# Optimization experiments

Measured on AMD Instinct MI355X. Metric: run time of the kernel, lower is better.

## Reference

```python
import jax, jax.numpy as jnp
import numpy as np

LNC = -1000000000.0
B, K, L, V, D = 64, 8, 256, 50257, 1024
EOS, PAD = 50256, 0
LENGTH_PENALTY = 1.0
EARLY_STOPPING = False


def _gather_beams(t, idx):
    # t: (B, old_beams, ...), idx: (B, new_beams) -> (B, new_beams, ...)
    idx = idx.reshape(idx.shape + (1,) * (t.ndim - 2))
    return jnp.take_along_axis(t, idx, axis=1)


def setup_inputs() -> dict:
    key = jax.random.key(0)
    ks = jax.random.split(key, 8)
    return dict(
        input_ids=jax.random.randint(ks[0], (B * K, 1), 0, V).astype(jnp.int32),
        sequences_state=jax.random.randint(ks[1], (B, K, L), 0, V).astype(jnp.int32),
        running_sequences_state=jax.random.randint(ks[2], (B, K, L), 0, V).astype(jnp.int32),
        log_probs_state=jax.random.normal(ks[3], (B, K), jnp.float32),
        running_log_probs_state=jax.random.normal(ks[4], (B, K), jnp.float32),
        is_finished_state=jax.random.randint(ks[5], (B, K), 0, 2).astype(jnp.int32),
        embed=jax.random.normal(ks[6], (V, D), jnp.float32) * 0.02,
        W=jax.random.normal(ks[7], (D, V), jnp.float32) * 0.02,
        absolute_step=17,
    )


def reference(input_ids, sequences_state, running_sequences_state, log_probs_state,
              running_log_probs_state, is_finished_state, embed, W, absolute_step):
    step = absolute_step  # static python int (current decode position)
    # mask selecting slot 0 for the freshly fed token
    mask = jnp.zeros((B, K, L), jnp.int32).at[:, :, 0].set(1)
    padded = jnp.pad(input_ids, ((0, 0), (0, L - 1))).reshape(B, K, L)
    running_sequences = mask * padded + (1 - mask) * running_sequences_state  # (B,K,L) int32

    # model: embedding lookup + LM head GEMM on the token at step-1
    model_input_ids = running_sequences[:, :, step - 1].reshape(B * K)
    logits = embed[model_input_ids] @ W                      # (B*K, V)
    log_probs = jax.nn.log_softmax(logits, axis=-1)          # logits_processor = identity
    log_probs = log_probs.reshape(B, K, V) + running_log_probs_state[:, :, None]
    flat = log_probs.reshape(B, K * V)

    beams_to_keep = 2 * K
    topk_log_probs, topk_indices = jax.lax.top_k(flat, beams_to_keep)  # (B,2K)
    topk_beam_indices = topk_indices // V
    topk_running_sequences = _gather_beams(running_sequences, topk_beam_indices)  # (B,2K,L)
    topk_ids = (topk_indices % V).astype(jnp.int32)
    topk_sequences = topk_running_sequences.at[:, :, step].set(topk_ids)

    did_finish = topk_sequences[:, :, step] == EOS           # (B,2K) bool
    running_topk_log_probs = topk_log_probs + did_finish * LNC
    next_topk_indices = jax.lax.top_k(running_topk_log_probs, K)[1]
    next_running_sequences = _gather_beams(topk_sequences, next_topk_indices)      # (B,K,L)
    next_running_log_probs = _gather_beams(running_topk_log_probs, next_topk_indices)

    topk_log_probs = topk_log_probs / (step ** LENGTH_PENALTY)
    full = jnp.all(is_finished_state.astype(bool), axis=-1, keepdims=True) & (EARLY_STOPPING is True)
    add_penalty = (~did_finish) | full
    topk_log_probs = topk_log_probs + add_penalty * LNC

    merged_sequences = jnp.concatenate([sequences_state, topk_sequences], axis=1)      # (B,3K,L)
    merged_log_probs = jnp.concatenate([log_probs_state, topk_log_probs], axis=1)      # (B,3K)
    merged_is_finished = jnp.concatenate([is_finished_state.astype(bool), did_finish], axis=1)
    topk_merged_indices = jax.lax.top_k(merged_log_probs, K)[1]
    next_sequences = _gather_beams(merged_sequences, topk_merged_indices)
    next_log_probs = _gather_beams(merged_log_probs, topk_merged_indices)
    next_is_finished = _gather_beams(merged_is_finished, topk_merged_indices)

    not_max_length_yet = step < L
    worst_finished = jnp.where(jnp.any(next_is_finished, axis=1),
                               jnp.min(log_probs_state, axis=1),
                               jnp.full((B,), LNC, jnp.float32))
    best_running = running_log_probs_state[:, 0] / (step ** LENGTH_PENALTY)
    improvement = jnp.any(best_running > worst_finished)
    still_open = ~(jnp.all(next_is_finished) & (EARLY_STOPPING is True))
    continue_search = not_max_length_yet & still_open & improvement

    none_finished = jnp.any(next_is_finished, axis=1)
    seqs = jnp.where(none_finished[:, None, None], next_sequences, next_running_sequences)
    generated_tokens = seqs[:, 0]                 # (B, L)
    done = ~continue_search
    return generated_tokens, done, next_log_probs, next_running_log_probs
```

## Files before the change

kernel.cpp:

```cpp
#include <hip/hip_runtime.h>
#include <cstdint>
#include <cstddef>

#define BB 64
#define KK 8
#define LL 256
#define VV 50257
#define DD 1024
#define EOS_TOK 50256
#define LNCf (-1000000000.0f)
#define NT 393
#define NCOL 50304
#define MAXT 400

typedef unsigned short ushort_t;
typedef __attribute__((ext_vector_type(4))) float f32x4;
typedef __attribute__((ext_vector_type(8))) short bf16x8;

struct __attribute__((packed, aligned(4))) f4u { float x, y, z, w; };

__device__ inline ushort_t bf16_rne(float x) {
    unsigned u = __float_as_uint(x);
    return (ushort_t)((u + 0x7fffu + ((u >> 16) & 1u)) >> 16);
}
__device__ inline float bf16_f32(ushort_t b) { return __uint_as_float(((unsigned)b) << 16); }

__global__ __launch_bounds__(256) void conv_aw(
    const float* __restrict__ embed, const int* __restrict__ input_ids,
    const int* __restrict__ rss, const int* __restrict__ step_p,
    ushort_t* __restrict__ At_hi, ushort_t* __restrict__ At_lo,
    const float* __restrict__ W, ushort_t* __restrict__ Wt)
{
    __shared__ ushort_t tile[64][66];
    const int bx = blockIdx.x;
    const int t = threadIdx.x;

    if (bx < 512) {
        const int r = bx;
        const int step = *step_p;
        const int tok = (step == 1) ? input_ids[r] : rss[r * LL + (step - 1)];
        f32x4 v = *(const f32x4*)(embed + (size_t)tok * DD + t * 4);
        ushort4 h, l;
        h.x = bf16_rne(v[0]); l.x = bf16_rne(v[0] - bf16_f32(h.x));
        h.y = bf16_rne(v[1]); l.y = bf16_rne(v[1] - bf16_f32(h.y));
        h.z = bf16_rne(v[2]); l.z = bf16_rne(v[2] - bf16_f32(h.z));
        h.w = bf16_rne(v[3]); l.w = bf16_rne(v[3] - bf16_f32(h.w));
        *(ushort4*)(At_hi + (size_t)r * DD + t * 4) = h;
        *(ushort4*)(At_lo + (size_t)r * DD + t * 4) = l;
        return;
    }

    const int b2 = bx - 512;
    const int k0 = (b2 & 15) * 64;
    const int n0 = (b2 >> 4) * 64;
    const int kr = t >> 4;
    const int nc = (t & 15) * 4;
#pragma unroll
    for (int j = 0; j < 4; ++j) {
        const int k = k0 + kr + j * 16;
        const int n = n0 + nc;
        const float* wp = W + (size_t)k * VV + n;
        float a, b3, c, d;
        if (n + 3 < VV) { f4u u = *(const f4u*)wp; a = u.x; b3 = u.y; c = u.z; d = u.w; }
        else {
            a  = (n     < VV) ? wp[0] : 0.f;
            b3 = (n + 1 < VV) ? wp[1] : 0.f;
            c  = (n + 2 < VV) ? wp[2] : 0.f;
            d  = (n + 3 < VV) ? wp[3] : 0.f;
        }
        tile[kr + j * 16][nc + 0] = bf16_rne(a);
        tile[kr + j * 16][nc + 1] = bf16_rne(b3);
        tile[kr + j * 16][nc + 2] = bf16_rne(c);
        tile[kr + j * 16][nc + 3] = bf16_rne(d);
    }
    __syncthreads();
    const int nr = t >> 2;
    const int kc = (t & 3) * 16;
    ushort_t vals[16];
#pragma unroll
    for (int j = 0; j < 16; ++j) vals[j] = tile[kc + j][nr];
    uint4 u0, u1;
    u0.x = vals[0] | ((unsigned)vals[1] << 16);  u0.y = vals[2] | ((unsigned)vals[3] << 16);
    u0.z = vals[4] | ((unsigned)vals[5] << 16);  u0.w = vals[6] | ((unsigned)vals[7] << 16);
    u1.x = vals[8] | ((unsigned)vals[9] << 16);  u1.y = vals[10] | ((unsigned)vals[11] << 16);
    u1.z = vals[12] | ((unsigned)vals[13] << 16); u1.w = vals[14] | ((unsigned)vals[15] << 16);
    ushort_t* op = Wt + (size_t)(n0 + nr) * DD + k0 + kc;
    *(uint4*)op = u0;
    *(uint4*)(op + 8) = u1;
}

__global__ __launch_bounds__(256) void gemm_full(
    const ushort_t* __restrict__ At_hi, const ushort_t* __restrict__ At_lo,
    const ushort_t* __restrict__ Wt, float* __restrict__ logits,
    float* __restrict__ msum)
{
    __shared__ ushort_t smem[24576];
    ushort_t* Ah = smem;
    ushort_t* Al = smem + 8192;
    ushort_t* Bs = smem + 16384;

    const int tid = threadIdx.x;
    const int wave = tid >> 6;
    const int lane = tid & 63;
    const int i = blockIdx.x;
    const int m_t = (i >> 3) & 3;
    const int n_t = (i & 7) + (((i >> 3) >> 2) << 3);
    if (n_t >= NT) return;
    const int m0 = m_t * 128;
    const int wm = wave >> 1, wn = wave & 1;
    const int fr = lane & 15;
    const int q  = lane >> 4;

    const int srow = lane >> 3;
    const int schunk = lane & 7;

    f32x4 acc[4][4];
#pragma unroll
    for (int a = 0; a < 4; ++a)
#pragma unroll
        for (int b = 0; b < 4; ++b)
#pragma unroll
            for (int e = 0; e < 4; ++e) acc[a][b][e] = 0.f;

    for (int t7 = 0; t7 < 16; ++t7) {
        const int kb = t7 * 64;
#pragma unroll
        for (int ii = 0; ii < 4; ++ii) {
            const int row = (ii * 4 + wave) * 8 + srow;
            const int soff = (schunk ^ (row & 7)) * 8;
            const ushort_t* srcH = At_hi + (size_t)(m0 + row) * DD + kb + soff;
            const ushort_t* srcL = At_lo + (size_t)(m0 + row) * DD + kb + soff;
            const ushort_t* srcB = Wt + (size_t)(n_t * 128 + row) * DD + kb + soff;
            __builtin_amdgcn_global_load_lds(
                (const __attribute__((address_space(1))) unsigned int*)srcH,
                (__attribute__((address_space(3))) unsigned int*)(Ah + (ii * 4 + wave) * 512),
                16, 0, 0);
            __builtin_amdgcn_global_load_lds(
                (const __attribute__((address_space(1))) unsigned int*)srcL,
                (__attribute__((address_space(3))) unsigned int*)(Al + (ii * 4 + wave) * 512),
                16, 0, 0);
            __builtin_amdgcn_global_load_lds(
                (const __attribute__((address_space(1))) unsigned int*)srcB,
                (__attribute__((address_space(3))) unsigned int*)(Bs + (ii * 4 + wave) * 512),
                16, 0, 0);
        }
        __syncthreads();
#pragma unroll
        for (int h = 0; h < 2; ++h) {
            bf16x8 b[4];
#pragma unroll
            for (int fn = 0; fn < 4; ++fn) {
                const int row = wn * 64 + fn * 16 + fr;
                const int off = ((h * 4 + q) ^ (row & 7)) * 16;
                b[fn] = *(const bf16x8*)((const char*)(Bs + row * 64) + off);
            }
#pragma unroll
            for (int fm = 0; fm < 4; ++fm) {
                const int row = wm * 64 + fm * 16 + fr;
                const int off = ((h * 4 + q) ^ (row & 7)) * 16;
                bf16x8 ah = *(const bf16x8*)((const char*)(Ah + row * 64) + off);
                bf16x8 al = *(const bf16x8*)((const char*)(Al + row * 64) + off);
#pragma unroll
                for (int fn = 0; fn < 4; ++fn) {
                    acc[fm][fn] = __builtin_amdgcn_mfma_f32_16x16x32_bf16(ah, b[fn], acc[fm][fn], 0, 0, 0);
                    acc[fm][fn] = __builtin_amdgcn_mfma_f32_16x16x32_bf16(al, b[fn], acc[fm][fn], 0, 0, 0);
                }
            }
        }
        __syncthreads();
    }

    const int n0 = n_t * 128;
    if (n0 + 128 > VV) {
        const int cgb = n0 + wn * 64 + fr;
#pragma unroll
        for (int fn = 0; fn < 4; ++fn)
            if (cgb + fn * 16 >= VV) {
#pragma unroll
                for (int fm = 0; fm < 4; ++fm)
#pragma unroll
                    for (int e = 0; e < 4; ++e) acc[fm][fn][e] = -INFINITY;
            }
    }

    const int crow0 = m0 + wm * 64 + q * 4;
    const int ccol0 = n0 + wn * 64 + fr;
#pragma unroll
    for (int fm = 0; fm < 4; ++fm)
#pragma unroll
        for (int fn = 0; fn < 4; ++fn) {
            const int col = ccol0 + fn * 16;
#pragma unroll
            for (int e = 0; e < 4; ++e)
                logits[(size_t)(crow0 + fm * 16 + e) * NCOL + col] = acc[fm][fn][e];
        }

    float* msb = (float*)smem;
#pragma unroll
    for (int fm = 0; fm < 4; ++fm)
#pragma unroll
        for (int e = 0; e < 4; ++e) {
            const float v0 = acc[fm][0][e], v1 = acc[fm][1][e];
            const float v2 = acc[fm][2][e], v3 = acc[fm][3][e];
            float vm = fmaxf(fmaxf(v0, v1), fmaxf(v2, v3));
#pragma unroll
            for (int sh = 1; sh < 16; sh <<= 1) vm = fmaxf(vm, __shfl_xor(vm, sh, 64));
            float vs = __expf(v0 - vm) + __expf(v1 - vm) + __expf(v2 - vm) + __expf(v3 - vm);
#pragma unroll
            for (int sh = 1; sh < 16; sh <<= 1) vs += __shfl_xor(vs, sh, 64);
            if (fr == 0) {
                const int row = wm * 64 + fm * 16 + q * 4 + e;
                msb[row * 4 + wn * 2]     = vm;
                msb[row * 4 + wn * 2 + 1] = vs;
            }
        }
    __syncthreads();
    if (tid < 128) {
        const float M0 = msb[tid * 4], S0 = msb[tid * 4 + 1];
        const float M1 = msb[tid * 4 + 2], S1 = msb[tid * 4 + 3];
        const float M = fmaxf(M0, M1);
        const float S = S0 * __expf(M0 - M) + S1 * __expf(M1 - M);
        const size_t p = (size_t)(m0 + tid) * NT + n_t;
        msum[p * 2] = M; msum[p * 2 + 1] = S;
    }
}

__global__ __launch_bounds__(64) void prune_scan(
    const float* __restrict__ msum, float* __restrict__ lse_out,
    int* __restrict__ tlist, int* __restrict__ tcount)
{
    const int r = blockIdx.x;
    const int lane = threadIdx.x;

    float m = -INFINITY, s = 0.f;
    float tv[16]; int tvi[16];
#pragma unroll
    for (int j = 0; j < 16; ++j) { tv[j] = -INFINITY; tvi[j] = 0x7fffffff; }

    for (int p = lane; p < NT; p += 64) {
        const size_t pb = (size_t)r * NT + p;
        const float M = msum[pb * 2], S = msum[pb * 2 + 1];
        const float mm = fmaxf(m, M);
        s = s * __expf(m - mm) + S * __expf(M - mm);
        m = mm;
        if (M > tv[15]) {
            float cv = M; int ci = p;
#pragma unroll
            for (int j = 0; j < 16; ++j) {
                const bool sw = (cv > tv[j]);
                const float tf = tv[j]; const int ti2 = tvi[j];
                if (sw) { tv[j] = cv; tvi[j] = ci; cv = tf; ci = ti2; }
            }
        }
    }
#pragma unroll
    for (int sh = 1; sh < 64; sh <<= 1) {
        const float m2 = __shfl_xor(m, sh, 64), s2 = __shfl_xor(s, sh, 64);
        const float mm = fmaxf(m, m2);
        s = s * __expf(m - mm) + s2 * __expf(m2 - mm);
        m = mm;
    }
    if (lane == 0) lse_out[r] = m + logf(s);

    unsigned used = 0;
    float T = -INFINITY;
#pragma unroll
    for (int t = 0; t < 16; ++t) {
        float bv = -INFINITY; int bi = 0x7fffffff;
#pragma unroll
        for (int j = 0; j < 16; ++j) {
            if (!((used >> j) & 1u) &&
                (tv[j] > bv || (tv[j] == bv && tvi[j] < bi))) { bv = tv[j]; bi = tvi[j]; }
        }
#pragma unroll
        for (int sh = 1; sh < 64; sh <<= 1) {
            const float v2 = __shfl_xor(bv, sh, 64);
            const int i2 = __shfl_xor(bi, sh, 64);
            if (v2 > bv || (v2 == bv && i2 < bi)) { bv = v2; bi = i2; }
        }
#pragma unroll
        for (int j = 0; j < 16; ++j)
            if (tvi[j] == bi) used |= 1u << j;
        T = bv;
    }

    __shared__ int cnt;
    if (lane == 0) cnt = 0;
    __syncthreads();
    for (int p = lane; p < NT; p += 64) {
        const float M = msum[((size_t)r * NT + p) * 2];
        if (M >= T) {
            const int slot = atomicAdd(&cnt, 1);
            tlist[r * MAXT + slot] = p;
        }
    }
    __syncthreads();
    if (lane == 0) tcount[r] = cnt;
}

__global__ __launch_bounds__(256) void topk_sparse(
    const float* __restrict__ logits, const int* __restrict__ tlist,
    const int* __restrict__ tcount, float* __restrict__ tv_out,
    int* __restrict__ ti_out)
{
    const int r = blockIdx.x;
    const int tid = threadIdx.x;
    const int cnt = tcount[r];

    float v[16]; int id[16];
#pragma unroll
    for (int j = 0; j < 16; ++j) { v[j] = -INFINITY; id[j] = 0x7fffffff; }

    const int total = cnt * 128;
    for (int idx = tid; idx < total; idx += 256) {
        const int tile = tlist[r * MAXT + (idx >> 7)];
        const int col = tile * 128 + (idx & 127);
        const float x = logits[(size_t)r * NCOL + col];
        if (x > v[15] || (x == v[15] && col < id[15])) {
            float cv = x; int ci = col;
#pragma unroll
            for (int j = 0; j < 16; ++j) {
                const bool sw = (cv > v[j]) || (cv == v[j] && ci < id[j]);
                const float tf = v[j]; const int ti2 = id[j];
                if (sw) { v[j] = cv; id[j] = ci; cv = tf; ci = ti2; }
            }
        }
    }

    __shared__ float mvv[256][17];
    __shared__ int mii[256][17];
#pragma unroll
    for (int j = 0; j < 16; ++j) { mvv[tid][j] = v[j]; mii[tid][j] = id[j]; }
    __syncthreads();

    auto level = [&](int st) {
        float nv[16]; int ni2[16];
        const float* av = mvv[tid];      const int* ai = mii[tid];
        const float* bv = mvv[tid + st]; const int* bi = mii[tid + st];
        int pa = 0, pb = 0;
#pragma unroll
        for (int o = 0; o < 16; ++o) {
            const float va = av[pa], vb2 = bv[pb];
            const int ia = ai[pa], ib = bi[pb];
            const bool ta = (va > vb2) || (va == vb2 && ia < ib);
            nv[o] = ta ? va : vb2;
            ni2[o] = ta ? ia : ib;
            pa += ta ? 1 : 0;
            pb += ta ? 0 : 1;
        }
#pragma unroll
        for (int j = 0; j < 16; ++j) { mvv[tid][j] = nv[j]; mii[tid][j] = ni2[j]; }
    };

    if (tid < 128) level(128);
    __syncthreads();
    if (tid < 64) {
        level(64); level(32); level(16); level(8); level(4); level(2); level(1);
        if (tid < 16) {
            tv_out[r * 16 + tid] = mvv[0][tid];
            ti_out[r * 16 + tid] = mii[0][tid];
        }
    }
}

__global__ __launch_bounds__(64) void beam_logic(
    const float* __restrict__ lse, const float* __restrict__ tv,
    const int* __restrict__ ti, const int* __restrict__ input_ids,
    const int* __restrict__ seq_state, const int* __restrict__ rss,
    const float* __restrict__ lps, const float* __restrict__ rlps,
    const int* __restrict__ isfin, const int* __restrict__ step_p,
    float* __restrict__ out, int* __restrict__ improve_ws)
{
    const int b = blockIdx.x;
    const int lane = threadIdx.x;
    const int kk = lane >> 3;
    const int r = b * KK + kk;

    const float off_r = rlps[r] - lse[r];

    const int s0 = (lane & 7) * 2;
    float cv[2]; int cidx[2];
#pragma unroll
    for (int mq = 0; mq < 2; ++mq) {
        cv[mq] = tv[r * 16 + s0 + mq] + off_r;
        cidx[mq] = kk * VV + ti[r * 16 + s0 + mq];
    }

    float wv[16]; int wi[16];
#pragma unroll
    for (int t = 0; t < 16; ++t) {
        float bv = cv[0]; int bi = cidx[0];
        if (cv[1] > bv || (cv[1] == bv && cidx[1] < bi)) { bv = cv[1]; bi = cidx[1]; }
#pragma unroll
        for (int sh = 1; sh < 64; sh <<= 1) {
            const float v2 = __shfl_xor(bv, sh, 64);
            const int i2 = __shfl_xor(bi, sh, 64);
            if (v2 > bv || (v2 == bv && i2 < bi)) { bv = v2; bi = i2; }
        }
        wv[t] = bv; wi[t] = bi;
#pragma unroll
        for (int mq = 0; mq < 2; ++mq)
            if (cidx[mq] == bi) { cv[mq] = -INFINITY; cidx[mq] = 0x7fffffff; }
    }

    int mode = 0, beam = 0, selk = 0, selv = 0, step = 0;
    if (lane == 0) {
        step = *step_p;
        const float stepf = (float)step;
        float runtl[16]; int tkk[16], tkid[16]; unsigned finmask = 0;
#pragma unroll
        for (int j = 0; j < 16; ++j) {
            tkk[j] = wi[j] / VV;
            tkid[j] = wi[j] - tkk[j] * VV;
            const bool f = (tkid[j] == EOS_TOK);
            finmask |= (f ? 1u : 0u) << j;
            runtl[j] = wv[j] + (f ? LNCf : 0.f);
        }
        unsigned used = 0;
        int selk_run = 0, selv_run = 0;
#pragma unroll
        for (int i2 = 0; i2 < 8; ++i2) {
            float bvv = 0.f; int bj = -1, bk = 0, bv2 = 0;
#pragma unroll
            for (int j = 0; j < 16; ++j) {
                if (!((used >> j) & 1u) && (bj < 0 || runtl[j] > bvv)) {
                    bvv = runtl[j]; bj = j; bk = tkk[j]; bv2 = tkid[j];
                }
            }
            used |= 1u << bj;
            out[BB * LL + 1 + BB * KK + b * KK + i2] = bvv;
            if (i2 == 0) { selk_run = bk; selv_run = bv2; }
        }
        float mvx[24]; unsigned mfinmask = 0;
#pragma unroll
        for (int j = 0; j < 8; ++j) {
            mvx[j] = lps[b * KK + j];
            mfinmask |= ((isfin[b * KK + j] != 0) ? 1u : 0u) << j;
        }
#pragma unroll
        for (int j = 0; j < 16; ++j) {
            const bool f = (finmask >> j) & 1u;
            mvx[8 + j] = wv[j] / stepf + (f ? 0.f : LNCf);
            mfinmask |= (f ? 1u : 0u) << (8 + j);
        }
        unsigned used2 = 0; int anyf = 0;
        int m0_state = 0, m0_beam = 0, m0_k = 0, m0_v = 0;
#pragma unroll
        for (int i2 = 0; i2 < 8; ++i2) {
            float bvv = 0.f; int bj = -1, bf = 0, bstate = 0, bbeam = 0, bk = 0, bv2 = 0;
#pragma unroll
            for (int j = 0; j < 24; ++j) {
                if (!((used2 >> j) & 1u) && (bj < 0 || mvx[j] > bvv)) {
                    bvv = mvx[j]; bj = j; bf = (mfinmask >> j) & 1u;
                    bstate = (j < 8) ? 1 : 0; bbeam = j;
                    bk = (j < 8) ? 0 : tkk[j - 8]; bv2 = (j < 8) ? 0 : tkid[j - 8];
                }
            }
            used2 |= 1u << bj;
            out[BB * LL + 1 + b * KK + i2] = bvv;
            anyf |= bf;
            if (i2 == 0) { m0_state = bstate; m0_beam = bbeam; m0_k = bk; m0_v = bv2; }
        }
        float worst = LNCf;
        if (anyf) {
            worst = lps[b * KK];
#pragma unroll
            for (int j = 1; j < 8; ++j) worst = fminf(worst, lps[b * KK + j]);
        }
        improve_ws[b] = ((rlps[b * KK] / stepf) > worst) ? 1 : 0;
        if (anyf) {
            if (m0_state) { mode = 0; beam = m0_beam; }
            else { mode = 1; selk = m0_k; selv = m0_v; }
        } else {
            mode = 1; selk = selk_run; selv = selv_run;
        }
    }
    mode = __shfl(mode, 0, 64);
    beam = __shfl(beam, 0, 64);
    selk = __shfl(selk, 0, 64);
    selv = __shfl(selv, 0, 64);
    step = __shfl(step, 0, 64);

#pragma unroll
    for (int it = 0; it < 4; ++it) {
        const int t2 = it * 64 + lane;
        int tokv;
        if (mode == 0) {
            tokv = seq_state[(b * KK + beam) * LL + t2];
        } else {
            tokv = (t2 == step) ? selv
                 : ((t2 == 0) ? input_ids[b * KK + selk]
                              : rss[(b * KK + selk) * LL + t2]);
        }
        out[b * LL + t2] = (float)tokv;
    }
}

__global__ __launch_bounds__(64) void finalize_done(
    const int* __restrict__ improve_ws, const int* __restrict__ step_p,
    float* __restrict__ out)
{
    int tid = threadIdx.x;
    bool imp = improve_ws[tid] != 0;
    bool any = __any(imp);
    if (tid == 0) {
        int step = *step_p;
        bool cont = (step < LL) && any;
        out[BB * LL] = cont ? 0.f : 1.f;
    }
}

extern "C" void kernel_launch(void* const* d_in, const int* in_sizes, int n_in,
                              void* d_out, int out_size, void* d_ws, size_t ws_size,
                              hipStream_t stream) {
    const int*   input_ids = (const int*)d_in[0];
    const int*   seq_state = (const int*)d_in[1];
    const int*   rss       = (const int*)d_in[2];
    const float* lps       = (const float*)d_in[3];
    const float* rlps      = (const float*)d_in[4];
    const int*   isfin     = (const int*)d_in[5];
    const float* embed     = (const float*)d_in[6];
    const float* W         = (const float*)d_in[7];
    const int*   step_p    = (const int*)d_in[8];
    float* out = (float*)d_out;

    char* ws = (char*)d_ws;
    size_t off = 0;
    auto alloc = [&](size_t bytes) { void* p = ws + off; off += (bytes + 255) & ~(size_t)255; return p; };
    ushort_t* Wt     = (ushort_t*)alloc((size_t)NCOL * DD * 2);
    float*    logits = (float*)alloc((size_t)512 * NCOL * 4);
    ushort_t* At_hi  = (ushort_t*)alloc((size_t)512 * DD * 2);
    ushort_t* At_lo  = (ushort_t*)alloc((size_t)512 * DD * 2);
    float*    msum   = (float*)alloc((size_t)512 * NT * 2 * 4);
    int*      tlist  = (int*)alloc((size_t)512 * MAXT * 4);
    int*      tcount = (int*)alloc(512 * 4);
    float*    lse    = (float*)alloc(512 * 4);
    float*    tvals  = (float*)alloc(512 * 16 * 4);
    int*      tidx   = (int*)alloc(512 * 16 * 4);
    int*      improw = (int*)alloc(64 * 4);
    (void)ws_size; (void)in_sizes; (void)n_in; (void)out_size;

    conv_aw<<<512 + 16 * 786, 256, 0, stream>>>(embed, input_ids, rss, step_p,
                                                At_hi, At_lo, W, Wt);
    gemm_full<<<1600, 256, 0, stream>>>(At_hi, At_lo, Wt, logits, msum);
    prune_scan<<<512, 64, 0, stream>>>(msum, lse, tlist, tcount);
    topk_sparse<<<512, 256, 0, stream>>>(logits, tlist, tcount, tvals, tidx);
    beam_logic<<<64, 64, 0, stream>>>(lse, tvals, tidx, input_ids, seq_state,
                                      rss, lps, rlps, isfin, step_p, out, improw);
    finalize_done<<<1, 64, 0, stream>>>(improw, step_p, out);
}
```

Measured before the change: 297.1 us.

## Fuse prune and top-k kernels, drop finalize kernel via atomic ticket

The GEMM epilogue now writes per-half-tile (max, sumexp) pairs straight to global memory, with no shared-memory reduction or extra barrier. The separate prune_scan and topk_sparse kernels become one prune_topk kernel. It keeps the candidate tile list in shared memory and builds it with ballot/popcount instead of atomics. The finalize_done kernel is removed: the last beam_logic block, found through an atomic ticket counter, computes the done flag. This cuts two launches and the global round trips for the tile list. The risks are that the ticket is never reset and relies on modulo 64, and that msum2 doubles in size.

```diff
diff --git a/kernel.cpp b/kernel.cpp
--- a/kernel.cpp
+++ b/kernel.cpp
@@ -92,7 +92,7 @@
 __global__ __launch_bounds__(256) void gemm_full(
     const ushort_t* __restrict__ At_hi, const ushort_t* __restrict__ At_lo,
     const ushort_t* __restrict__ Wt, float* __restrict__ logits,
-    float* __restrict__ msum)
+    float* __restrict__ msum2)
 {
     __shared__ ushort_t smem[24576];
     ushort_t* Ah = smem;
@@ -195,7 +195,6 @@
                 logits[(size_t)(crow0 + fm * 16 + e) * NCOL + col] = acc[fm][fn][e];
         }
 
-    float* msb = (float*)smem;
 #pragma unroll
     for (int fm = 0; fm < 4; ++fm)
 #pragma unroll
@@ -209,111 +208,106 @@
 #pragma unroll
             for (int sh = 1; sh < 16; sh <<= 1) vs += __shfl_xor(vs, sh, 64);
             if (fr == 0) {
-                const int row = wm * 64 + fm * 16 + q * 4 + e;
-                msb[row * 4 + wn * 2]     = vm;
-                msb[row * 4 + wn * 2 + 1] = vs;
-            }
-        }
-    __syncthreads();
-    if (tid < 128) {
-        const float M0 = msb[tid * 4], S0 = msb[tid * 4 + 1];
-        const float M1 = msb[tid * 4 + 2], S1 = msb[tid * 4 + 3];
-        const float M = fmaxf(M0, M1);
-        const float S = S0 * __expf(M0 - M) + S1 * __expf(M1 - M);
-        const size_t p = (size_t)(m0 + tid) * NT + n_t;
-        msum[p * 2] = M; msum[p * 2 + 1] = S;
-    }
+                const int row = m0 + wm * 64 + fm * 16 + q * 4 + e;
+                float2 p; p.x = vm; p.y = vs;
+                *(float2*)&msum2[((size_t)row * NT + n_t) * 4 + wn * 2] = p;
+            }
+        }
 }
 
-__global__ __launch_bounds__(64) void prune_scan(
-    const float* __restrict__ msum, float* __restrict__ lse_out,
-    int* __restrict__ tlist, int* __restrict__ tcount)
-{
-    const int r = blockIdx.x;
-    const int lane = threadIdx.x;
-
-    float m = -INFINITY, s = 0.f;
-    float tv[16]; int tvi[16];
-#pragma unroll
-    for (int j = 0; j < 16; ++j) { tv[j] = -INFINITY; tvi[j] = 0x7fffffff; }
-
-    for (int p = lane; p < NT; p += 64) {
-        const size_t pb = (size_t)r * NT + p;
-        const float M = msum[pb * 2], S = msum[pb * 2 + 1];
-        const float mm = fmaxf(m, M);
-        s = s * __expf(m - mm) + S * __expf(M - mm);
-        m = mm;
-        if (M > tv[15]) {
-            float cv = M; int ci = p;
-#pragma unroll
-            for (int j = 0; j < 16; ++j) {
-                const bool sw = (cv > tv[j]);
-                const float tf = tv[j]; const int ti2 = tvi[j];
-                if (sw) { tv[j] = cv; tvi[j] = ci; cv = tf; ci = ti2; }
-            }
-        }
-    }
-#pragma unroll
-    for (int sh = 1; sh < 64; sh <<= 1) {
-        const float m2 = __shfl_xor(m, sh, 64), s2 = __shfl_xor(s, sh, 64);
-        const float mm = fmaxf(m, m2);
-        s = s * __expf(m - mm) + s2 * __expf(m2 - mm);
-        m = mm;
-    }
-    if (lane == 0) lse_out[r] = m + logf(s);
-
-    unsigned used = 0;
-    float T = -INFINITY;
-#pragma unroll
-    for (int t = 0; t < 16; ++t) {
-        float bv = -INFINITY; int bi = 0x7fffffff;
-#pragma unroll
-        for (int j = 0; j < 16; ++j) {
-            if (!((used >> j) & 1u) &&
-                (tv[j] > bv || (tv[j] == bv && tvi[j] < bi))) { bv = tv[j]; bi = tvi[j]; }
-        }
-#pragma unroll
-        for (int sh = 1; sh < 64; sh <<= 1) {
-            const float v2 = __shfl_xor(bv, sh, 64);
-            const int i2 = __shfl_xor(bi, sh, 64);
-            if (v2 > bv || (v2 == bv && i2 < bi)) { bv = v2; bi = i2; }
-        }
-#pragma unroll
-        for (int j = 0; j < 16; ++j)
-            if (tvi[j] == bi) used |= 1u << j;
-        T = bv;
-    }
-
-    __shared__ int cnt;
-    if (lane == 0) cnt = 0;
-    __syncthreads();
-    for (int p = lane; p < NT; p += 64) {
-        const float M = msum[((size_t)r * NT + p) * 2];
-        if (M >= T) {
-            const int slot = atomicAdd(&cnt, 1);
-            tlist[r * MAXT + slot] = p;
-        }
-    }
-    __syncthreads();
-    if (lane == 0) tcount[r] = cnt;
-}
-
-__global__ __launch_bounds__(256) void topk_sparse(
-    const float* __restrict__ logits, const int* __restrict__ tlist,
-    const int* __restrict__ tcount, float* __restrict__ tv_out,
+__global__ __launch_bounds__(256) void prune_topk(
+    const float* __restrict__ msum2, const float* __restrict__ logits,
+    float* __restrict__ lse_out, float* __restrict__ tv_out,
     int* __restrict__ ti_out)
 {
     const int r = blockIdx.x;
     const int tid = threadIdx.x;
-    const int cnt = tcount[r];
-
+
+    __shared__ int s_tlist[MAXT];
+    __shared__ int s_cnt;
+
+    if (tid < 64) {
+        const int lane = tid;
+        float m = -INFINITY, s = 0.f;
+        float tv[16]; int tvi[16];
+#pragma unroll
+        for (int j = 0; j < 16; ++j) { tv[j] = -INFINITY; tvi[j] = 0x7fffffff; }
+
+        for (int p = lane; p < NT; p += 64) {
+            const f32x4 qv = *(const f32x4*)&msum2[((size_t)r * NT + p) * 4];
+            float mm = fmaxf(m, qv[0]);
+            s = s * __expf(m - mm) + qv[1] * __expf(qv[0] - mm);
+            m = mm;
+            mm = fmaxf(m, qv[2]);
+            s = s * __expf(m - mm) + qv[3] * __expf(qv[2] - mm);
+            m = mm;
+            const float tmax = fmaxf(qv[0], qv[2]);
+            if (tmax > tv[15]) {
+                float cv = tmax; int ci = p;
+#pragma unroll
+                for (int j = 0; j < 16; ++j) {
+                    const bool sw = (cv > tv[j]);
+                    const float tf = tv[j]; const int ti2 = tvi[j];
+                    if (sw) { tv[j] = cv; tvi[j] = ci; cv = tf; ci = ti2; }
+                }
+            }
+        }
+#pragma unroll
+        for (int sh = 1; sh < 64; sh <<= 1) {
+            const float m2 = __shfl_xor(m, sh, 64), s2 = __shfl_xor(s, sh, 64);
+            const float mm = fmaxf(m, m2);
+            s = s * __expf(m - mm) + s2 * __expf(m2 - mm);
+            m = mm;
+        }
+        if (lane == 0) lse_out[r] = m + logf(s);
+
+        unsigned used = 0;
+        float T = -INFINITY;
+#pragma unroll
+        for (int t = 0; t < 16; ++t) {
+            float bv = -INFINITY; int bi = 0x7fffffff;
+#pragma unroll
+            for (int j = 0; j < 16; ++j) {
+                if (!((used >> j) & 1u) &&
+                    (tv[j] > bv || (tv[j] == bv && tvi[j] < bi))) { bv = tv[j]; bi = tvi[j]; }
+            }
+#pragma unroll
+            for (int sh = 1; sh < 64; sh <<= 1) {
+                const float v2 = __shfl_xor(bv, sh, 64);
+                const int i2 = __shfl_xor(bi, sh, 64);
+                if (v2 > bv || (v2 == bv && i2 < bi)) { bv = v2; bi = i2; }
+            }
+#pragma unroll
+            for (int j = 0; j < 16; ++j)
+                if (tvi[j] == bi) used |= 1u << j;
+            T = bv;
+        }
+
+        const unsigned long long lmask_lt = (1ULL << lane) - 1ULL;
+        int base = 0;
+        for (int it = 0; it < 7; ++it) {
+            const int p = it * 64 + lane;
+            bool pred = false;
+            if (p < NT) {
+                const f32x4 qv = *(const f32x4*)&msum2[((size_t)r * NT + p) * 4];
+                pred = fmaxf(qv[0], qv[2]) >= T;
+            }
+            const unsigned long long mask = __ballot(pred);
+            if (pred) s_tlist[base + __popcll(mask & lmask_lt)] = p;
+            base += __popcll(mask);
+        }
+        if (lane == 0) s_cnt = base;
+    }
+    __syncthreads();
+
+    const int cnt = s_cnt;
     float v[16]; int id[16];
 #pragma unroll
     for (int j = 0; j < 16; ++j) { v[j] = -INFINITY; id[j] = 0x7fffffff; }
 
     const int total = cnt * 128;
     for (int idx = tid; idx < total; idx += 256) {
-        const int tile = tlist[r * MAXT + (idx >> 7)];
+        const int tile = s_tlist[idx >> 7];
         const int col = tile * 128 + (idx & 127);
         const float x = logits[(size_t)r * NCOL + col];
         if (x > v[15] || (x == v[15] && col < id[15])) {
@@ -369,7 +363,8 @@
     const int* __restrict__ seq_state, const int* __restrict__ rss,
     const float* __restrict__ lps, const float* __restrict__ rlps,
     const int* __restrict__ isfin, const int* __restrict__ step_p,
-    float* __restrict__ out, int* __restrict__ improve_ws)
+    float* __restrict__ out, int* __restrict__ improve_ws,
+    unsigned* __restrict__ ticket)
 {
     const int b = blockIdx.x;
     const int lane = threadIdx.x;
@@ -494,19 +489,18 @@
         }
         out[b * LL + t2] = (float)tokv;
     }
-}
-
-__global__ __launch_bounds__(64) void finalize_done(
-    const int* __restrict__ improve_ws, const int* __restrict__ step_p,
-    float* __restrict__ out)
-{
-    int tid = threadIdx.x;
-    bool imp = improve_ws[tid] != 0;
-    bool any = __any(imp);
-    if (tid == 0) {
-        int step = *step_p;
-        bool cont = (step < LL) && any;
-        out[BB * LL] = cont ? 0.f : 1.f;
+
+    __threadfence();
+    if (lane == 0) {
+        const unsigned slot = atomicAdd(ticket, 1u);
+        if ((slot & 63u) == 63u) {
+            __threadfence();
+            int any = 0;
+#pragma unroll
+            for (int j = 0; j < BB; ++j) any |= improve_ws[j];
+            const bool cont = (step < LL) && (any != 0);
+            out[BB * LL] = cont ? 0.f : 1.f;
+        }
     }
 }
 
@@ -531,21 +525,19 @@
     float*    logits = (float*)alloc((size_t)512 * NCOL * 4);
     ushort_t* At_hi  = (ushort_t*)alloc((size_t)512 * DD * 2);
     ushort_t* At_lo  = (ushort_t*)alloc((size_t)512 * DD * 2);
-    float*    msum   = (float*)alloc((size_t)512 * NT * 2 * 4);
-    int*      tlist  = (int*)alloc((size_t)512 * MAXT * 4);
-    int*      tcount = (int*)alloc(512 * 4);
+    float*    msum2  = (float*)alloc((size_t)512 * NT * 4 * 4);
     float*    lse    = (float*)alloc(512 * 4);
     float*    tvals  = (float*)alloc(512 * 16 * 4);
     int*      tidx   = (int*)alloc(512 * 16 * 4);
     int*      improw = (int*)alloc(64 * 4);
+    unsigned* ticket = (unsigned*)alloc(4);
     (void)ws_size; (void)in_sizes; (void)n_in; (void)out_size;
 
     conv_aw<<<512 + 16 * 786, 256, 0, stream>>>(embed, input_ids, rss, step_p,
                                                 At_hi, At_lo, W, Wt);
-    gemm_full<<<1600, 256, 0, stream>>>(At_hi, At_lo, Wt, logits, msum);
-    prune_scan<<<512, 64, 0, stream>>>(msum, lse, tlist, tcount);
-    topk_sparse<<<512, 256, 0, stream>>>(logits, tlist, tcount, tvals, tidx);
+    gemm_full<<<1600, 256, 0, stream>>>(At_hi, At_lo, Wt, logits, msum2);
+    prune_topk<<<512, 256, 0, stream>>>(msum2, logits, lse, tvals, tidx);
     beam_logic<<<64, 64, 0, stream>>>(lse, tvals, tidx, input_ids, seq_state,
-                                      rss, lps, rlps, isfin, step_p, out, improw);
-    finalize_done<<<1, 64, 0, stream>>>(improw, step_p, out);
+                                      rss, lps, rlps, isfin, step_p, out,
+                                      improw, ticket);
 }
```

Result: faster. 290.0 us (-2.4%).
